# Kernel optimization log

Measured on AMD Instinct MI355X. Metric: run time of the kernel, lower is better.

Reference implementation:

```python
import jax, jax.numpy as jnp
import numpy as np

B, D, N, K = 16, 128, 4096, 1024


def setup_inputs() -> dict:
    key = jax.random.key(0)
    k1, k2 = jax.random.split(key)
    ze = jax.random.normal(k1, (B, D, N), dtype=jnp.float32)
    emb = jax.random.normal(k2, (K, D), dtype=jnp.float32)
    return {"ze": ze, "emb": emb}


def reference(ze, emb):
    """VQ forward: nearest-codebook quantization with straight-through estimator.

    ze:  (B, D, N) encoder latents (D = n_latent_dim, N = timesteps)
    emb: (K, D) codebook (stop-gradient applied, matching StopGrad on emb)
    returns zq_rg: (B, D, N) quantized latents; gradient flows straight to ze
    (ReplaceGrad: zq gets zero grad, ze gets the output grad).
    """
    emb_sg = jax.lax.stop_gradient(emb)
    # Squared L2 distance via expansion, avoiding the (B, D, K, N) broadcast:
    # d2[b,k,n] = ||ze[b,:,n]||^2 + ||emb[k]||^2 - 2 <ze[b,:,n], emb[k]>
    ze_sq = jnp.sum(ze * ze, axis=1)            # (B, N)
    emb_sq = jnp.sum(emb_sg * emb_sg, axis=1)   # (K,)
    dot = jnp.einsum('bdn,kd->bkn', ze, emb_sg)  # (B, K, N)
    d2 = ze_sq[:, None, :] + emb_sq[None, :, None] - 2.0 * dot
    ind = jnp.argmin(d2, axis=1)                # (B, N) nearest codebook index
    zq = jnp.transpose(jnp.take(emb_sg, ind, axis=0), (0, 2, 1))  # (B, D, N)
    # ReplaceGrad straight-through: value of zq, gradient routed to ze.
    zq_rg = ze + jax.lax.stop_gradient(zq - ze)
    return zq_rg
```

## Files before the change

kernel.cpp:

```cpp
#include <hip/hip_runtime.h>
#include <hip/hip_bf16.h>
#include <math.h>

#define BB 16
#define DD 128
#define NN 4096
#define KK 1024
#define CADD 320.0f
#define TAU 0.45f

typedef __attribute__((ext_vector_type(8))) short short8;
typedef __attribute__((ext_vector_type(4))) float f32x4;

static __device__ __forceinline__ unsigned short f32_bf16_rne(float f) {
    unsigned u = __float_as_uint(f);
    u += 0x7FFF + ((u >> 16) & 1);
    return (unsigned short)(u >> 16);
}
static __device__ __forceinline__ unsigned umin32(unsigned a, unsigned b) { return a < b ? a : b; }
static __device__ __forceinline__ unsigned umax32(unsigned a, unsigned b) { return a > b ? a : b; }
static __device__ __forceinline__ unsigned umed3(unsigned a, unsigned b, unsigned c) {
    unsigned d;
    asm("v_med3_u32 %0, %1, %2, %3" : "=v"(d) : "v"(a), "v"(b), "v"(c));
    return d;
}

__global__ void emb_sq_kernel(const float* __restrict__ emb,
                              float* __restrict__ e2) {
    int k = blockIdx.x * 256 + threadIdx.x;
    if (k >= KK) return;
    const float4* row = reinterpret_cast<const float4*>(emb + (size_t)k * DD);
    float a0 = 0.f, a1 = 0.f, a2 = 0.f, a3 = 0.f;
#pragma unroll
    for (int i = 0; i < DD / 16; ++i) {
        float4 v0 = row[i * 4 + 0];
        float4 v1 = row[i * 4 + 1];
        float4 v2 = row[i * 4 + 2];
        float4 v3 = row[i * 4 + 3];
        a0 += v0.x * v0.x + v0.y * v0.y + v0.z * v0.z + v0.w * v0.w;
        a1 += v1.x * v1.x + v1.y * v1.y + v1.z * v1.z + v1.w * v1.w;
        a2 += v2.x * v2.x + v2.y * v2.y + v2.z * v2.z + v2.w * v2.w;
        a3 += v3.x * v3.x + v3.y * v3.y + v3.z * v3.z + v3.w * v3.w;
    }
    e2[k] = (a0 + a1) + (a2 + a3) + CADD;
}

__global__ void emb_pack_kernel(const float* __restrict__ emb,
                                short* __restrict__ epk) {
    int g = blockIdx.x * 256 + threadIdx.x;
    int lane = g & 63;
    int s    = (g >> 6) & 3;
    int t    = g >> 8;
    int k = t * 16 + (lane & 15);
    int d = s * 32 + ((lane >> 4) & 3) * 8;
    const float* src = emb + (size_t)k * DD + d;
    short8 h;
#pragma unroll
    for (int j = 0; j < 8; ++j) h[j] = (short)f32_bf16_rne(-2.0f * src[j]);
    *reinterpret_cast<short8*>(epk + (size_t)g * 8) = h;
}

#define CEU(a, b) { unsigned lo_ = umin32(a, b), hi_ = umax32(a, b); (a) = lo_; (b) = hi_; }
#define MRG9(A1, A2, A3, A4, B1, B2, B3, B4) \
    CEU(A1, B1) CEU(A2, B2) CEU(A3, B3) CEU(A4, B4) \
    CEU(A3, B1) CEU(A4, B2) \
    CEU(A2, A3) \
    CEU(A4, B1) \
    CEU(A3, A4)

__global__ __launch_bounds__(256, 4)
void vq_mfma(const float* __restrict__ ze, const float* __restrict__ emb,
             const short* __restrict__ epk, const float* __restrict__ e2,
             float* __restrict__ out) {
    __shared__ __align__(16) char ubuf[(DD + 1) * 32 * 4];
    __shared__ unsigned kbuf[4][32][4];
    __shared__ int winner_s[32];
    __shared__ int rlist[32];
    __shared__ int rcnt;

    short* zstage = reinterpret_cast<short*>(ubuf);

    const int tid  = threadIdx.x;
    const int lane = tid & 63;
    const int wave = tid >> 6;
    const int b    = blockIdx.x >> 7;
    const int n0b  = (blockIdx.x & 127) * 32;
    const float* zb = ze + (size_t)b * DD * NN;

    const int nq = lane & 15;
    const int dq = (lane >> 4) & 3;

#pragma unroll
    for (int cg = 0; cg < 2; ++cg) {
        const int col = n0b + cg * 16 + nq;
        const int d0  = wave * 32 + dq * 8;
        const float* zp = zb + (size_t)d0 * NN + col;
        short8 h;
#pragma unroll
        for (int j = 0; j < 8; ++j) h[j] = (short)f32_bf16_rne(zp[(size_t)j * NN]);
        *reinterpret_cast<short8*>(zstage + (cg * 256 + wave * 64 + lane) * 8) = h;
    }
    __syncthreads();

    short8 zf[2][4];
#pragma unroll
    for (int cg = 0; cg < 2; ++cg)
#pragma unroll
        for (int s = 0; s < 4; ++s)
            zf[cg][s] = *reinterpret_cast<const short8*>(
                zstage + ((cg * 4 + s) * 64 + lane) * 8);
    __syncthreads();

    unsigned K1[2], K2[2];
    K1[0] = K1[1] = K2[0] = K2[1] = 0xFFFFFFFFu;

    const int t0 = wave * 16;
    const short* ep  = epk + (size_t)(t0 * 4) * 512 + (size_t)lane * 8;
    const float* e2p = e2 + t0 * 16 + dq * 4;
    unsigned kb = (unsigned)(t0 * 16 + dq * 4);

    short8 aC0 = *reinterpret_cast<const short8*>(ep);
    short8 aC1 = *reinterpret_cast<const short8*>(ep + 512);
    short8 aC2 = *reinterpret_cast<const short8*>(ep + 1024);
    short8 aC3 = *reinterpret_cast<const short8*>(ep + 1536);
    float4 evC = *reinterpret_cast<const float4*>(e2p);

#pragma unroll 4
    for (int tt = 0; tt < 16; ++tt) {
        short8 aN0, aN1, aN2, aN3; float4 evN;
        if (tt < 15) {
            aN0 = *reinterpret_cast<const short8*>(ep + 2048);
            aN1 = *reinterpret_cast<const short8*>(ep + 2560);
            aN2 = *reinterpret_cast<const short8*>(ep + 3072);
            aN3 = *reinterpret_cast<const short8*>(ep + 3584);
            evN = *reinterpret_cast<const float4*>(e2p + 16);
        }

        f32x4 acc0 = {evC.x, evC.y, evC.z, evC.w};
        f32x4 acc1 = acc0;
#define STEP(AF, S) \
        acc0 = __builtin_amdgcn_mfma_f32_16x16x32_bf16(AF, zf[0][S], acc0, 0, 0, 0); \
        acc1 = __builtin_amdgcn_mfma_f32_16x16x32_bf16(AF, zf[1][S], acc1, 0, 0, 0);
        STEP(aC0, 0) STEP(aC1, 1) STEP(aC2, 2) STEP(aC3, 3)
#undef STEP

#pragma unroll
        for (int cg = 0; cg < 2; ++cg) {
            const f32x4 a = (cg == 0) ? acc0 : acc1;
#pragma unroll
            for (int r = 0; r < 4; ++r) {
                const unsigned x = (__float_as_uint(a[r]) & 0xFFFFFC00u) | (kb + r);
                K2[cg] = umed3(K1[cg], K2[cg], x);
                K1[cg] = umin32(K1[cg], x);
            }
        }
        kb += 16; ep += 2048; e2p += 16;
        aC0 = aN0; aC1 = aN1; aC2 = aN2; aC3 = aN3; evC = evN;
    }

    unsigned T1[2], T2[2], T3[2], T4[2];
#pragma unroll
    for (int cg = 0; cg < 2; ++cg) {
        unsigned A1 = K1[cg], A2 = K2[cg];
        unsigned B1 = __shfl_xor(A1, 16);
        unsigned B2 = __shfl_xor(A2, 16);
        CEU(A1, B1) CEU(A2, B2) CEU(A2, B1)
        unsigned C1 = __shfl_xor(A1, 32);
        unsigned C2 = __shfl_xor(A2, 32);
        unsigned C3 = __shfl_xor(B1, 32);
        unsigned C4 = __shfl_xor(B2, 32);
        MRG9(A1, A2, B1, B2, C1, C2, C3, C4)
        T1[cg] = A1; T2[cg] = A2; T3[cg] = B1; T4[cg] = B2;
    }

    if (lane < 32) {
        const int cgid = lane >> 4;
        kbuf[wave][lane][0] = cgid ? T1[1] : T1[0];
        kbuf[wave][lane][1] = cgid ? T2[1] : T2[0];
        kbuf[wave][lane][2] = cgid ? T3[1] : T3[0];
        kbuf[wave][lane][3] = cgid ? T4[1] : T4[0];
    }
    __syncthreads();

    if (wave == 0) {
        const int c = lane & 31;
        unsigned A1 = kbuf[0][c][0], A2 = kbuf[0][c][1];
        unsigned A3 = kbuf[0][c][2], A4 = kbuf[0][c][3];
#pragma unroll
        for (int q = 1; q < 4; ++q) {
            unsigned B1 = kbuf[q][c][0], B2 = kbuf[q][c][1];
            unsigned B3 = kbuf[q][c][2], B4 = kbuf[q][c][3];
            MRG9(A1, A2, A3, A4, B1, B2, B3, B4)
        }
        const float M1 = __uint_as_float(A1 & 0xFFFFFC00u);
        const float M2 = __uint_as_float(A2 & 0xFFFFFC00u);
        const bool trig = (lane < 32) && ((M2 - M1) < TAU);
        if (lane < 32) {
            winner_s[c] = (int)(A1 & 0x3FFu);
            kbuf[0][c][0] = A1; kbuf[0][c][1] = A2;
            kbuf[0][c][2] = A3; kbuf[0][c][3] = A4;
        }
        const unsigned long long mask = __ballot(trig);
        if (trig) {
            const int idx = __popcll(mask & ((1ull << lane) - 1ull));
            rlist[idx] = c;
        }
        if (lane == 0) rcnt = (int)__popcll(mask);
    }
    __syncthreads();

    {
        const int rc = rcnt;
        for (int j = wave; j < rc; j += 4) {
            const int c = rlist[j];
            const int coln = n0b + c;
            const int I0 = (int)(kbuf[0][c][0] & 0x3FFu);
            const int I1 = (int)(kbuf[0][c][1] & 0x3FFu);
            const int I2 = (int)(kbuf[0][c][2] & 0x3FFu);
            const int I3 = (int)(kbuf[0][c][3] & 0x3FFu);
            double s0 = 0.0, s1 = 0.0, s2 = 0.0, s3 = 0.0;
#pragma unroll
            for (int h = 0; h < 2; ++h) {
                const int d = h * 64 + lane;
                const double zv = (double)zb[(size_t)d * NN + coln];
                double q;
                q = zv - (double)emb[(size_t)I0 * DD + d]; s0 += q * q;
                q = zv - (double)emb[(size_t)I1 * DD + d]; s1 += q * q;
                q = zv - (double)emb[(size_t)I2 * DD + d]; s2 += q * q;
                q = zv - (double)emb[(size_t)I3 * DD + d]; s3 += q * q;
            }
#pragma unroll
            for (int off = 1; off < 64; off <<= 1) {
                s0 += __shfl_xor(s0, off);
                s1 += __shfl_xor(s1, off);
                s2 += __shfl_xor(s2, off);
                s3 += __shfl_xor(s3, off);
            }
            int best = I0; double db = s0;
            if (s1 < db || (s1 == db && I1 < best)) { db = s1; best = I1; }
            if (s2 < db || (s2 == db && I2 < best)) { db = s2; best = I2; }
            if (s3 < db || (s3 == db && I3 < best)) { db = s3; best = I3; }
            if (lane == 0) winner_s[c] = best;
        }
    }
    __syncthreads();

    float (*ew)[DD + 1] = reinterpret_cast<float(*)[DD + 1]>(ubuf);
#pragma unroll 2
    for (int rr = 0; rr < 8; ++rr) {
        const int r = wave * 8 + rr;
        const int idx = winner_s[r];
        ew[r][lane]      = emb[(size_t)idx * DD + lane];
        ew[r][lane + 64] = emb[(size_t)idx * DD + lane + 64];
    }
    __syncthreads();

    {
        const int c = lane & 31;
        const int coln = n0b + c;
#pragma unroll 4
        for (int dd = 0; dd < 16; ++dd) {
            const int d = wave * 32 + dd * 2 + (lane >> 5);
            const float zv = zb[(size_t)d * NN + coln];
            const float evv = ew[c][d];
            out[((size_t)b * DD + d) * NN + coln] = zv + (evv - zv);
        }
    }
}

extern "C" void kernel_launch(void* const* d_in, const int* in_sizes, int n_in,
                              void* d_out, int out_size, void* d_ws, size_t ws_size,
                              hipStream_t stream) {
    (void)in_sizes; (void)n_in; (void)out_size; (void)ws_size;
    const float* ze  = (const float*)d_in[0];
    const float* emb = (const float*)d_in[1];
    float*       out = (float*)d_out;

    char* ws = (char*)d_ws;
    short* epk = (short*)ws;
    float* e2  = (float*)(ws + (size_t)KK * DD * 2);

    emb_sq_kernel<<<KK / 256, 256, 0, stream>>>(emb, e2);
    emb_pack_kernel<<<(KK * DD / 8) / 256, 256, 0, stream>>>(emb, epk);
    vq_mfma<<<(BB * NN) / 32, 256, 0, stream>>>(ze, emb, epk, e2, out);
}
```

Before: 49.06 us.

## Widen per-block column tile to 64 to reuse codebook fragments across more columns

Each block now handles 64 columns instead of 32, so every codebook fragment loaded from the packed embedding feeds four MFMA column groups instead of two, halving total codebook traffic and halving the block count. The explicit register double-buffering of the next codebook tile is dropped in favour of plain loads inside a loop unrolled by 2. The change raises register and LDS use per block, which may lower occupancy under the launch bound of 4, and the final merge and output phases are reshaped to cover 64 columns.

```diff
diff --git a/kernel.cpp b/kernel.cpp
--- a/kernel.cpp
+++ b/kernel.cpp
@@ -72,10 +72,10 @@
 void vq_mfma(const float* __restrict__ ze, const float* __restrict__ emb,
              const short* __restrict__ epk, const float* __restrict__ e2,
              float* __restrict__ out) {
-    __shared__ __align__(16) char ubuf[(DD + 1) * 32 * 4];
-    __shared__ unsigned kbuf[4][32][4];
-    __shared__ int winner_s[32];
-    __shared__ int rlist[32];
+    __shared__ __align__(16) char ubuf[(DD + 1) * 64 * 4];
+    __shared__ unsigned kbuf[4][64][4];
+    __shared__ int winner_s[64];
+    __shared__ int rlist[64];
     __shared__ int rcnt;
 
     short* zstage = reinterpret_cast<short*>(ubuf);
@@ -83,15 +83,15 @@
     const int tid  = threadIdx.x;
     const int lane = tid & 63;
     const int wave = tid >> 6;
-    const int b    = blockIdx.x >> 7;
-    const int n0b  = (blockIdx.x & 127) * 32;
+    const int b    = blockIdx.x >> 6;
+    const int n0b  = (blockIdx.x & 63) * 64;
     const float* zb = ze + (size_t)b * DD * NN;
 
     const int nq = lane & 15;
     const int dq = (lane >> 4) & 3;
 
 #pragma unroll
-    for (int cg = 0; cg < 2; ++cg) {
+    for (int cg = 0; cg < 4; ++cg) {
         const int col = n0b + cg * 16 + nq;
         const int d0  = wave * 32 + dq * 8;
         const float* zp = zb + (size_t)d0 * NN + col;
@@ -102,51 +102,46 @@
     }
     __syncthreads();
 
-    short8 zf[2][4];
-#pragma unroll
-    for (int cg = 0; cg < 2; ++cg)
+    short8 zf[4][4];
+#pragma unroll
+    for (int cg = 0; cg < 4; ++cg)
 #pragma unroll
         for (int s = 0; s < 4; ++s)
             zf[cg][s] = *reinterpret_cast<const short8*>(
                 zstage + ((cg * 4 + s) * 64 + lane) * 8);
     __syncthreads();
 
-    unsigned K1[2], K2[2];
-    K1[0] = K1[1] = K2[0] = K2[1] = 0xFFFFFFFFu;
+    unsigned K1[4], K2[4];
+#pragma unroll
+    for (int cg = 0; cg < 4; ++cg) { K1[cg] = K2[cg] = 0xFFFFFFFFu; }
 
     const int t0 = wave * 16;
     const short* ep  = epk + (size_t)(t0 * 4) * 512 + (size_t)lane * 8;
     const float* e2p = e2 + t0 * 16 + dq * 4;
     unsigned kb = (unsigned)(t0 * 16 + dq * 4);
 
-    short8 aC0 = *reinterpret_cast<const short8*>(ep);
-    short8 aC1 = *reinterpret_cast<const short8*>(ep + 512);
-    short8 aC2 = *reinterpret_cast<const short8*>(ep + 1024);
-    short8 aC3 = *reinterpret_cast<const short8*>(ep + 1536);
-    float4 evC = *reinterpret_cast<const float4*>(e2p);
-
-#pragma unroll 4
+#pragma unroll 2
     for (int tt = 0; tt < 16; ++tt) {
-        short8 aN0, aN1, aN2, aN3; float4 evN;
-        if (tt < 15) {
-            aN0 = *reinterpret_cast<const short8*>(ep + 2048);
-            aN1 = *reinterpret_cast<const short8*>(ep + 2560);
-            aN2 = *reinterpret_cast<const short8*>(ep + 3072);
-            aN3 = *reinterpret_cast<const short8*>(ep + 3584);
-            evN = *reinterpret_cast<const float4*>(e2p + 16);
-        }
-
-        f32x4 acc0 = {evC.x, evC.y, evC.z, evC.w};
-        f32x4 acc1 = acc0;
+        const short8 a0 = *reinterpret_cast<const short8*>(ep);
+        const short8 a1 = *reinterpret_cast<const short8*>(ep + 512);
+        const short8 a2 = *reinterpret_cast<const short8*>(ep + 1024);
+        const short8 a3 = *reinterpret_cast<const short8*>(ep + 1536);
+        const float4 ev = *reinterpret_cast<const float4*>(e2p);
+
+        f32x4 acc0 = {ev.x, ev.y, ev.z, ev.w};
+        f32x4 acc1 = acc0, acc2 = acc0, acc3 = acc0;
 #define STEP(AF, S) \
         acc0 = __builtin_amdgcn_mfma_f32_16x16x32_bf16(AF, zf[0][S], acc0, 0, 0, 0); \
-        acc1 = __builtin_amdgcn_mfma_f32_16x16x32_bf16(AF, zf[1][S], acc1, 0, 0, 0);
-        STEP(aC0, 0) STEP(aC1, 1) STEP(aC2, 2) STEP(aC3, 3)
+        acc1 = __builtin_amdgcn_mfma_f32_16x16x32_bf16(AF, zf[1][S], acc1, 0, 0, 0); \
+        acc2 = __builtin_amdgcn_mfma_f32_16x16x32_bf16(AF, zf[2][S], acc2, 0, 0, 0); \
+        acc3 = __builtin_amdgcn_mfma_f32_16x16x32_bf16(AF, zf[3][S], acc3, 0, 0, 0);
+        STEP(a0, 0) STEP(a1, 1) STEP(a2, 2) STEP(a3, 3)
 #undef STEP
 
 #pragma unroll
-        for (int cg = 0; cg < 2; ++cg) {
-            const f32x4 a = (cg == 0) ? acc0 : acc1;
+        for (int cg = 0; cg < 4; ++cg) {
+            const f32x4 a = (cg == 0) ? acc0 : (cg == 1) ? acc1
+                          : (cg == 2) ? acc2 : acc3;
 #pragma unroll
             for (int r = 0; r < 4; ++r) {
                 const unsigned x = (__float_as_uint(a[r]) & 0xFFFFFC00u) | (kb + r);
@@ -155,12 +150,11 @@
             }
         }
         kb += 16; ep += 2048; e2p += 16;
-        aC0 = aN0; aC1 = aN1; aC2 = aN2; aC3 = aN3; evC = evN;
-    }
-
-    unsigned T1[2], T2[2], T3[2], T4[2];
-#pragma unroll
-    for (int cg = 0; cg < 2; ++cg) {
+    }
+
+    unsigned T1[4], T2[4], T3[4], T4[4];
+#pragma unroll
+    for (int cg = 0; cg < 4; ++cg) {
         unsigned A1 = K1[cg], A2 = K2[cg];
         unsigned B1 = __shfl_xor(A1, 16);
         unsigned B2 = __shfl_xor(A2, 16);
@@ -173,17 +167,19 @@
         T1[cg] = A1; T2[cg] = A2; T3[cg] = B1; T4[cg] = B2;
     }
 
-    if (lane < 32) {
+    {
         const int cgid = lane >> 4;
-        kbuf[wave][lane][0] = cgid ? T1[1] : T1[0];
-        kbuf[wave][lane][1] = cgid ? T2[1] : T2[0];
-        kbuf[wave][lane][2] = cgid ? T3[1] : T3[0];
-        kbuf[wave][lane][3] = cgid ? T4[1] : T4[0];
+#define SEL4(T) ((cgid & 2) ? ((cgid & 1) ? T[3] : T[2]) : ((cgid & 1) ? T[1] : T[0]))
+        kbuf[wave][lane][0] = SEL4(T1);
+        kbuf[wave][lane][1] = SEL4(T2);
+        kbuf[wave][lane][2] = SEL4(T3);
+        kbuf[wave][lane][3] = SEL4(T4);
+#undef SEL4
     }
     __syncthreads();
 
     if (wave == 0) {
-        const int c = lane & 31;
+        const int c = lane;
         unsigned A1 = kbuf[0][c][0], A2 = kbuf[0][c][1];
         unsigned A3 = kbuf[0][c][2], A4 = kbuf[0][c][3];
 #pragma unroll
@@ -194,12 +190,10 @@
         }
         const float M1 = __uint_as_float(A1 & 0xFFFFFC00u);
         const float M2 = __uint_as_float(A2 & 0xFFFFFC00u);
-        const bool trig = (lane < 32) && ((M2 - M1) < TAU);
-        if (lane < 32) {
-            winner_s[c] = (int)(A1 & 0x3FFu);
-            kbuf[0][c][0] = A1; kbuf[0][c][1] = A2;
-            kbuf[0][c][2] = A3; kbuf[0][c][3] = A4;
-        }
+        const bool trig = (M2 - M1) < TAU;
+        winner_s[c] = (int)(A1 & 0x3FFu);
+        kbuf[0][c][0] = A1; kbuf[0][c][1] = A2;
+        kbuf[0][c][2] = A3; kbuf[0][c][3] = A4;
         const unsigned long long mask = __ballot(trig);
         if (trig) {
             const int idx = __popcll(mask & ((1ull << lane) - 1ull));
@@ -246,9 +240,9 @@
     __syncthreads();
 
     float (*ew)[DD + 1] = reinterpret_cast<float(*)[DD + 1]>(ubuf);
-#pragma unroll 2
-    for (int rr = 0; rr < 8; ++rr) {
-        const int r = wave * 8 + rr;
+#pragma unroll 4
+    for (int rr = 0; rr < 16; ++rr) {
+        const int r = wave * 16 + rr;
         const int idx = winner_s[r];
         ew[r][lane]      = emb[(size_t)idx * DD + lane];
         ew[r][lane + 64] = emb[(size_t)idx * DD + lane + 64];
@@ -256,13 +250,12 @@
     __syncthreads();
 
     {
-        const int c = lane & 31;
-        const int coln = n0b + c;
+        const int coln = n0b + lane;
 #pragma unroll 4
-        for (int dd = 0; dd < 16; ++dd) {
-            const int d = wave * 32 + dd * 2 + (lane >> 5);
+        for (int dd = 0; dd < 32; ++dd) {
+            const int d = wave * 32 + dd;
             const float zv = zb[(size_t)d * NN + coln];
-            const float evv = ew[c][d];
+            const float evv = ew[lane][d];
             out[((size_t)b * DD + d) * NN + coln] = zv + (evv - zv);
         }
     }
@@ -282,5 +275,5 @@
 
     emb_sq_kernel<<<KK / 256, 256, 0, stream>>>(emb, e2);
     emb_pack_kernel<<<(KK * DD / 8) / 256, 256, 0, stream>>>(emb, epk);
-    vq_mfma<<<(BB * NN) / 32, 256, 0, stream>>>(ze, emb, epk, e2, out);
-}
+    vq_mfma<<<(BB * NN) / 64, 256, 0, stream>>>(ze, emb, epk, e2, out);
+}
```

Result: faster. 45.29 us (-7.7%).
